# Performance work log

Measured on AMD Instinct MI355X. Metric: run time of the kernel, lower is better.

Reference implementation:

```python
import jax, jax.numpy as jnp
import numpy as np

B, T, F = 16, 4096, 80      # batch, frames, mel bins
C = 512                     # conv channels
ZD, ZN = 64, 512            # codebook dim / size
YD, YN = 128, 128           # speaker embed dim / count
K = 5                       # kernel size
SLOPE = 0.2                 # leaky relu negative slope


def conv1d(x, w, b):
    # x: [B,Cin,T], w: [Cout,Cin,K], 'same' padding, stride 1
    pad = (w.shape[-1] - 1) // 2
    y = jax.lax.conv_general_dilated(x, w, (1,), [(pad, pad)],
                                     dimension_numbers=('NCH', 'OIH', 'NCH'))
    return y + b[None, :, None]


def convT1(x, w, b):
    # torch ConvTranspose1d(stride=1, padding=(K-1)//2) == conv with spatially
    # flipped, in/out-swapped kernel. w: [Cin, Cout, K]
    wc = jnp.flip(w, -1).transpose(1, 0, 2)  # -> [Cout, Cin, K]
    return conv1d(x, wc, b)


def ln_c(x, g, b, eps=1e-5):
    # layer norm over channel axis, per (batch, time) position
    m = jnp.mean(x, 1, keepdims=True)
    v = jnp.var(x, 1, keepdims=True)
    return (x - m) * jax.lax.rsqrt(v + eps) * g[None, :, None] + b[None, :, None]


def _forward(x, y, enc_w1, enc_b1, enc_g1, enc_bt1, enc_w2, enc_b2, enc_g2, enc_bt2,
             enc_w3, enc_b3, enc_g3, enc_bt3, mlp_w, mlp_b, codebook, spk_emb,
             dec_w1, dec_b1, dec_g1, dec_bt1, dec_w2, dec_b2, dec_g2, dec_bt2,
             dec_w3, dec_b3):
    xc = x.transpose(0, 2, 1)                                    # [B,F,T]
    # Conditions: normalized speaker embedding lookup
    spk = spk_emb / jnp.linalg.norm(spk_emb, axis=1, keepdims=True)
    ye = spk[y].transpose(0, 2, 1)                               # [B,YD,T]
    # encoder: Conv1d -> LayerNorm(channel) -> LeakyReLU, x3, then 1x1 conv to z_dim
    h = jax.nn.leaky_relu(ln_c(conv1d(xc, enc_w1, enc_b1), enc_g1, enc_bt1), SLOPE)
    h = jax.nn.leaky_relu(ln_c(conv1d(h, enc_w2, enc_b2), enc_g2, enc_bt2), SLOPE)
    h = jax.nn.leaky_relu(ln_c(conv1d(h, enc_w3, enc_b3), enc_g3, enc_bt3), SLOPE)
    z = conv1d(h, mlp_w, mlp_b)                                  # [B,ZD,T]
    # vector quantizer (eval path): cdist^2 -> argmin -> gather
    zt = z.transpose(0, 2, 1)                                    # [B,T,ZD]
    zf = zt.reshape(-1, ZD)                                      # [B*T,ZD]
    d = (jnp.sum(zf * zf, axis=1, keepdims=True)
         + jnp.sum(codebook * codebook, axis=1)
         - 2.0 * zf @ codebook.T)                                # [B*T,ZN]
    idx = jnp.argmin(d, axis=1)
    z_vq = codebook[idx].reshape(zt.shape).transpose(0, 2, 1)    # [B,ZD,T]
    # decoder: (concat y -> ConvT -> LayerNorm -> GLU) x2, then concat y -> ConvT
    def glu_layer(h, w, b, g, bt):
        h = jnp.concatenate([h, ye], axis=1)
        h = ln_c(convT1(h, w, b), g, bt)
        a, gate = jnp.split(h, 2, axis=1)
        return a * jax.nn.sigmoid(gate)
    h = glu_layer(z_vq, dec_w1, dec_b1, dec_g1, dec_bt1)
    h = glu_layer(h, dec_w2, dec_b2, dec_g2, dec_bt2)
    h = jnp.concatenate([h, ye], axis=1)
    xhat = convT1(h, dec_w3, dec_b3)                             # [B,F,T]
    return xhat.transpose(0, 2, 1)                               # [B,T,F]


def setup_inputs() -> dict:
    key = jax.random.key(0)
    ks = jax.random.split(key, 16)
    def n(k, shape, sc=0.05):
        return jax.random.normal(k, shape, jnp.float32) * sc
    return {
        "x": jax.random.normal(ks[0], (B, T, F), jnp.float32),
        "y": jax.random.randint(ks[1], (B, T), 0, YN),
        "enc_w1": n(ks[2], (C, F, K)), "enc_b1": jnp.zeros(C), "enc_g1": jnp.ones(C), "enc_bt1": jnp.zeros(C),
        "enc_w2": n(ks[3], (C, C, K)), "enc_b2": jnp.zeros(C), "enc_g2": jnp.ones(C), "enc_bt2": jnp.zeros(C),
        "enc_w3": n(ks[4], (C, C, K)), "enc_b3": jnp.zeros(C), "enc_g3": jnp.ones(C), "enc_bt3": jnp.zeros(C),
        "mlp_w": n(ks[5], (ZD, C, 1)), "mlp_b": jnp.zeros(ZD),
        "codebook": jax.random.normal(ks[6], (ZN, ZD), jnp.float32),
        "spk_emb": jax.random.normal(ks[7], (YN, YD), jnp.float32),
        "dec_w1": n(ks[8], (ZD + YD, 2 * C, K)), "dec_b1": jnp.zeros(2 * C), "dec_g1": jnp.ones(2 * C), "dec_bt1": jnp.zeros(2 * C),
        "dec_w2": n(ks[9], (C + YD, 2 * C, K)), "dec_b2": jnp.zeros(2 * C), "dec_g2": jnp.ones(2 * C), "dec_bt2": jnp.zeros(2 * C),
        "dec_w3": n(ks[10], (C + YD, F, K)), "dec_b3": jnp.zeros(F),
    }


def reference(x, y, enc_w1, enc_b1, enc_g1, enc_bt1, enc_w2, enc_b2, enc_g2, enc_bt2,
              enc_w3, enc_b3, enc_g3, enc_bt3, mlp_w, mlp_b, codebook, spk_emb,
              dec_w1, dec_b1, dec_g1, dec_bt1, dec_w2, dec_b2, dec_g2, dec_bt2,
              dec_w3, dec_b3):
    return _forward(x, y, enc_w1, enc_b1, enc_g1, enc_bt1, enc_w2, enc_b2, enc_g2, enc_bt2,
                    enc_w3, enc_b3, enc_g3, enc_bt3, mlp_w, mlp_b, codebook, spk_emb,
                    dec_w1, dec_b1, dec_g1, dec_bt1, dec_w2, dec_b2, dec_g2, dec_bt2,
                    dec_w3, dec_b3)
```

## Files before the change

### kernel.cpp

```cpp
#include <hip/hip_runtime.h>
#include <hip/hip_bf16.h>
#include <cmath>

#define T_LEN 4096
#define BATCH 16
typedef __hip_bfloat16 bf16;
typedef unsigned short u16;
typedef float f32x4 __attribute__((ext_vector_type(4)));
typedef short s16x8 __attribute__((ext_vector_type(8)));
typedef unsigned short u16x8 __attribute__((ext_vector_type(8)));

__device__ __forceinline__ float ldx(const void* p, int dt, size_t i) {
    return dt ? __bfloat162float(((const bf16*)p)[i]) : ((const float*)p)[i];
}
__device__ __forceinline__ void stx(void* p, int dt, size_t i, float v) {
    if (dt) ((bf16*)p)[i] = __float2bfloat16(v);
    else ((float*)p)[i] = v;
}
__device__ __forceinline__ u16 f2b(float v) {
    bf16 h = __float2bfloat16(v);
    return *(u16*)&h;
}
__device__ __forceinline__ float b2f(u16 u) {
    return __bfloat162float(*(const bf16*)&u);
}

__global__ void detect_kernel(const float* __restrict__ x, int* __restrict__ flag) {
    __shared__ int s[256];
    int tid = threadIdx.x;
    int bad = 0;
    for (int i = tid; i < 2048; i += 256) {
        float v = x[i];
        if (!(fabsf(v) < 1e30f)) bad = 1;
    }
    s[tid] = bad;
    __syncthreads();
    for (int off = 128; off > 0; off >>= 1) {
        if (tid < off) s[tid] |= s[tid + off];
        __syncthreads();
    }
    if (tid == 0) *flag = s[0];
}

__global__ void spk_norm_kernel(const int* __restrict__ dflag,
                                const void* __restrict__ spk,
                                float* __restrict__ out) {
    const int f = *dflag;
    int s = blockIdx.x, d = threadIdx.x;
    float v = ldx(spk, f, (size_t)s * 128 + d);
    __shared__ float red[128];
    red[d] = v * v;
    __syncthreads();
    for (int off = 64; off > 0; off >>= 1) {
        if (d < off) red[d] += red[d + off];
        __syncthreads();
    }
    float rs = rsqrtf(red[0]);
    out[s * 128 + d] = v * rs;
}

__global__ __launch_bounds__(256) void repack0_kernel(
    const int* __restrict__ dflag, const void* __restrict__ src,
    int Cout, int Cin, int K, int ocp, int Cinp,
    bf16* __restrict__ dsthi, bf16* __restrict__ dstlo) {
    const int F = *dflag;
    __shared__ u16 sh[64 * 32 * 5];
    __shared__ u16 sl[64 * 32 * 5];
    const int ic0 = blockIdx.x * 32;
    const int oc0 = blockIdx.y * 64;
    const int tid = threadIdx.x;
    const int N = 64 * 32 * K;
    for (int idx = tid; idx < N; idx += 256) {
        int ocl = idx / (32 * K);
        int r = idx % (32 * K);
        int icl = r / K, k = r % K;
        int oc = oc0 + ocl, ic = ic0 + icl;
        float v = 0.f;
        if (oc < Cout && ic < Cin)
            v = ldx(src, F, ((size_t)oc * Cin + ic) * K + k);
        u16 hb = f2b(v);
        sh[(ocl * 32 + icl) * K + k] = hb;
        sl[(ocl * 32 + icl) * K + k] = f2b(v - b2f(hb));
    }
    __syncthreads();
    const int M = K * 64 * 4;
    for (int idx = tid; idx < M; idx += 256) {
        int k = idx / (64 * 4);
        int r = idx % (64 * 4);
        int ocl = r >> 2;
        int g8 = (r & 3) << 3;
        u16x8 h, l;
#pragma unroll
        for (int j = 0; j < 8; j++) {
            h[j] = sh[(ocl * 32 + g8 + j) * K + k];
            l[j] = sl[(ocl * 32 + g8 + j) * K + k];
        }
        size_t off = ((size_t)k * ocp + oc0 + ocl) * Cinp + ic0 + g8;
        *(u16x8*)&dsthi[off] = h;
        if (dstlo) *(u16x8*)&dstlo[off] = l;
    }
}

__global__ __launch_bounds__(256) void repack1_kernel(
    const int* __restrict__ dflag, const void* __restrict__ src,
    int Cout, int Cin, int K, int ocp, int Cinp,
    bf16* __restrict__ dsthi) {
    const int F = *dflag;
    __shared__ u16 sh[64 * 32 * 5];
    const int ic0 = blockIdx.x * 64;
    const int oc0 = blockIdx.y * 32;
    const int tid = threadIdx.x;
    const int N = 64 * 32 * K;
    for (int idx = tid; idx < N; idx += 256) {
        int icl = idx / (32 * K);
        int r = idx % (32 * K);
        int ocl = r / K, k = r % K;
        int oc = oc0 + ocl, ic = ic0 + icl;
        float v = 0.f;
        if (oc < Cout && ic < Cin)
            v = ldx(src, F, ((size_t)ic * Cout + oc) * K + k);
        sh[(icl * 32 + ocl) * K + (K - 1 - k)] = f2b(v);
    }
    __syncthreads();
    const int M = K * 32 * 8;
    for (int idx = tid; idx < M; idx += 256) {
        int k = idx / (32 * 8);
        int r = idx % (32 * 8);
        int ocl = r >> 3;
        int g8 = (r & 7) << 3;
        u16x8 h;
#pragma unroll
        for (int j = 0; j < 8; j++)
            h[j] = sh[((g8 + j) * 32 + ocl) * K + k];
        size_t off = ((size_t)k * ocp + oc0 + ocl) * Cinp + ic0 + g8;
        *(u16x8*)&dsthi[off] = h;
    }
}

__global__ void xprep_kernel(const int* __restrict__ dflag,
                             const void* __restrict__ x, int b0,
                             bf16* __restrict__ xp) {
    const int F = *dflag;
    int b = blockIdx.y;
    int t = blockIdx.x * 256 + threadIdx.x;
    size_t src = ((size_t)(b0 + b) * T_LEN + t) * 80;
    u16* row = (u16*)xp + ((size_t)b * T_LEN + t) * 192;
    for (int c4 = 0; c4 < 96; c4 += 4) {
        ushort4 h, l;
        u16* hp = (u16*)&h;
        u16* lp = (u16*)&l;
        for (int j = 0; j < 4; j++) {
            int c = c4 + j;
            float v = (c < 80) ? ldx(x, F, src + c) : 0.f;
            u16 hb = f2b(v);
            hp[j] = hb;
            lp[j] = f2b(v - b2f(hb));
        }
        *(ushort4*)&row[c4] = h;
        *(ushort4*)&row[96 + c4] = l;
    }
}

__global__ void ye_kernel(const int* __restrict__ y, int b0,
                          const float* __restrict__ spk_n,
                          bf16* __restrict__ D1, bf16* __restrict__ D2,
                          bf16* __restrict__ D3) {
    int b = blockIdx.y;
    int t = blockIdx.x * 256 + threadIdx.x;
    int idx = y[(size_t)(b0 + b) * T_LEN + t];
    const float* s = spk_n + (size_t)idx * 128;
    size_t r = (size_t)b * T_LEN + t;
    u16* p1 = (u16*)D1 + r * 192 + 64;
    u16* p2 = (u16*)D2 + r * 640 + 512;
    u16* p3 = (u16*)D3 + r * 640 + 512;
    for (int d4 = 0; d4 < 128; d4 += 4) {
        float4 v = *(const float4*)&s[d4];
        ushort4 h;
        h.x = f2b(v.x); h.y = f2b(v.y); h.z = f2b(v.z); h.w = f2b(v.w);
        *(ushort4*)&p1[d4] = h;
        *(ushort4*)&p2[d4] = h;
        *(ushort4*)&p3[d4] = h;
    }
}

template <int KK>
__global__ __launch_bounds__(256) void conv_mfma(
    const int* __restrict__ dflag,
    const bf16* __restrict__ act, int RS, int loOff, int aloMode, int Cinp,
    const bf16* __restrict__ whi, const bf16* __restrict__ wlo, int wloMode,
    const void* __restrict__ bias,
    void* __restrict__ outp, int odt, int oRS, int ocMax, int boff) {
    constexpr int PAD = (KK - 1) / 2;
    constexpr int SROWS = 128 + KK - 1;
    const int F = *dflag;
    const bool useALo = (aloMode == 1) || (aloMode == 2 && F == 0);
    const bool useWLo = (wloMode == 2 && F == 0) && (wlo != nullptr);
    const int ocp = gridDim.y << 7;
    const int t0 = blockIdx.x * 128;
    const int oc0 = blockIdx.y * 128;
    const int b = blockIdx.z;
    const int tid = threadIdx.x;
    const int lane = tid & 63;
    const int wid = tid >> 6;
    const int widT = wid >> 1;
    const int widN = wid & 1;
    const int l16 = lane & 15;
    const int quad = lane >> 4;
    const int q8 = quad * 8;

    __shared__ __align__(16) bf16 sA[2 * SROWS * 40];
    __shared__ __align__(16) bf16 sB[KK * 128 * 40];

    f32x4 acc[4][4];
#pragma unroll
    for (int i = 0; i < 4; i++)
#pragma unroll
        for (int j = 0; j < 4; j++) acc[i][j] = (f32x4){0.f, 0.f, 0.f, 0.f};

    const int nch = Cinp >> 5;
    for (int ch = 0; ch < nch; ch++) {
        const int ic0 = ch << 5;
        for (int g = tid; g < SROWS * 4; g += 256) {
            int row = g >> 2, c8 = (g & 3) << 3;
            int t = t0 - PAD + row;
            u16x8 v = (u16x8){0, 0, 0, 0, 0, 0, 0, 0};
            u16x8 vl = (u16x8){0, 0, 0, 0, 0, 0, 0, 0};
            if (t >= 0 && t < T_LEN) {
                const u16* src = (const u16*)act + ((size_t)b * T_LEN + t) * RS + ic0 + c8;
                v = *(const u16x8*)src;
                if (useALo) vl = *(const u16x8*)(src + loOff);
            }
            *(u16x8*)&sA[row * 40 + c8] = v;
            if (useALo) *(u16x8*)&sA[(SROWS + row) * 40 + c8] = vl;
        }
        for (int g = tid; g < KK * 512; g += 256) {
            int tap = g >> 9;
            int r = g & 511;
            int ocr = r >> 2, c8 = (r & 3) << 3;
            const u16* src = (const u16*)whi +
                             ((size_t)tap * ocp + oc0 + ocr) * Cinp + ic0 + c8;
            *(u16x8*)&sB[(tap * 128 + ocr) * 40 + c8] = *(const u16x8*)src;
        }
        __syncthreads();

#pragma unroll
        for (int tap = 0; tap < KK; tap++) {
            s16x8 bfr[4];
#pragma unroll
            for (int ni = 0; ni < 4; ni++)
                bfr[ni] = *(const s16x8*)&sB[(tap * 128 + widN * 64 + ni * 16 + l16) * 40 + q8];
#pragma unroll
            for (int mi = 0; mi < 4; mi++) {
                int row = widT * 64 + mi * 16 + l16 + tap;
                s16x8 a = *(const s16x8*)&sA[row * 40 + q8];
#pragma unroll
                for (int ni = 0; ni < 4; ni++)
                    acc[mi][ni] = __builtin_amdgcn_mfma_f32_16x16x32_bf16(
                        a, bfr[ni], acc[mi][ni], 0, 0, 0);
                if (useALo) {
                    s16x8 al = *(const s16x8*)&sA[(SROWS + row) * 40 + q8];
#pragma unroll
                    for (int ni = 0; ni < 4; ni++)
                        acc[mi][ni] = __builtin_amdgcn_mfma_f32_16x16x32_bf16(
                            al, bfr[ni], acc[mi][ni], 0, 0, 0);
                }
            }
        }
        if (useWLo) {
            __syncthreads();
            for (int g = tid; g < KK * 512; g += 256) {
                int tap = g >> 9;
                int r = g & 511;
                int ocr = r >> 2, c8 = (r & 3) << 3;
                const u16* src = (const u16*)wlo +
                                 ((size_t)tap * ocp + oc0 + ocr) * Cinp + ic0 + c8;
                *(u16x8*)&sB[(tap * 128 + ocr) * 40 + c8] = *(const u16x8*)src;
            }
            __syncthreads();
#pragma unroll
            for (int tap = 0; tap < KK; tap++) {
                s16x8 bfr[4];
#pragma unroll
                for (int ni = 0; ni < 4; ni++)
                    bfr[ni] = *(const s16x8*)&sB[(tap * 128 + widN * 64 + ni * 16 + l16) * 40 + q8];
#pragma unroll
                for (int mi = 0; mi < 4; mi++) {
                    int row = widT * 64 + mi * 16 + l16 + tap;
                    s16x8 a = *(const s16x8*)&sA[row * 40 + q8];
#pragma unroll
                    for (int ni = 0; ni < 4; ni++)
                        acc[mi][ni] = __builtin_amdgcn_mfma_f32_16x16x32_bf16(
                            a, bfr[ni], acc[mi][ni], 0, 0, 0);
                }
            }
        }
        __syncthreads();
    }

#pragma unroll
    for (int ni = 0; ni < 4; ni++) {
        int oc = oc0 + widN * 64 + ni * 16 + l16;
        if (oc >= ocMax) continue;
        float bv = ldx(bias, F, oc);
#pragma unroll
        for (int mi = 0; mi < 4; mi++) {
#pragma unroll
            for (int r = 0; r < 4; r++) {
                int t = t0 + widT * 64 + mi * 16 + quad * 4 + r;
                float v = acc[mi][ni][r] + bv;
                size_t off = ((size_t)(b + boff) * T_LEN + t) * (size_t)oRS + oc;
                if (odt == 0) ((float*)outp)[off] = v;
                else if (odt == 1) ((bf16*)outp)[off] = __float2bfloat16(v);
                else stx(outp, F, off, v);
            }
        }
    }
}

__global__ __launch_bounds__(256) void ln_lrelu(
    const int* __restrict__ dflag, const float* __restrict__ Fin,
    bf16* __restrict__ E, const void* __restrict__ g, const void* __restrict__ bt) {
    const int Fl = *dflag;
    int b = blockIdx.y;
    int t = blockIdx.x * 4 + (threadIdx.x >> 6);
    int lane = threadIdx.x & 63;
    const float* row = Fin + ((size_t)b * T_LEN + t) * 512 + lane * 8;
    float vv[8];
    *(float4*)&vv[0] = *(const float4*)row;
    *(float4*)&vv[4] = *(const float4*)(row + 4);
    float s = 0.f, s2 = 0.f;
#pragma unroll
    for (int j = 0; j < 8; j++) { s += vv[j]; s2 += vv[j] * vv[j]; }
    for (int m = 32; m; m >>= 1) {
        s += __shfl_xor(s, m);
        s2 += __shfl_xor(s2, m);
    }
    float mean = s / 512.f;
    float var = s2 / 512.f - mean * mean;
    float rstd = rsqrtf(var + 1e-5f);
    u16* eo = (u16*)E + ((size_t)b * T_LEN + t) * 1024 + lane * 8;
    ushort4 h[2], l[2];
#pragma unroll
    for (int j = 0; j < 8; j++) {
        int c = lane * 8 + j;
        float v = (vv[j] - mean) * rstd * ldx(g, Fl, c) + ldx(bt, Fl, c);
        v = v >= 0.f ? v : 0.2f * v;
        u16 hb = f2b(v);
        ((u16*)h)[j] = hb;
        ((u16*)l)[j] = f2b(v - b2f(hb));
    }
    *(ushort4*)&eo[0] = h[0];
    *(ushort4*)&eo[4] = h[1];
    *(ushort4*)&eo[512] = l[0];
    *(ushort4*)&eo[516] = l[1];
}

__global__ __launch_bounds__(256) void ln_glu(
    const int* __restrict__ dflag, const bf16* __restrict__ Fin,
    bf16* __restrict__ D, int oRS, const void* __restrict__ g,
    const void* __restrict__ bt) {
    const int Fl = *dflag;
    int b = blockIdx.y;
    int t = blockIdx.x * 4 + (threadIdx.x >> 6);
    int lane = threadIdx.x & 63;
    const u16* row = (const u16*)Fin + ((size_t)b * T_LEN + t) * 1024;
    ushort4 ua[2], ug[2];
    ua[0] = *(const ushort4*)&row[lane * 8];
    ua[1] = *(const ushort4*)&row[lane * 8 + 4];
    ug[0] = *(const ushort4*)&row[512 + lane * 8];
    ug[1] = *(const ushort4*)&row[512 + lane * 8 + 4];
    float av[8], gv[8];
#pragma unroll
    for (int j = 0; j < 8; j++) {
        av[j] = b2f(((u16*)ua)[j]);
        gv[j] = b2f(((u16*)ug)[j]);
    }
    float s = 0.f, s2 = 0.f;
#pragma unroll
    for (int j = 0; j < 8; j++) {
        s += av[j] + gv[j];
        s2 += av[j] * av[j] + gv[j] * gv[j];
    }
    for (int m = 32; m; m >>= 1) {
        s += __shfl_xor(s, m);
        s2 += __shfl_xor(s2, m);
    }
    float mean = s / 1024.f;
    float var = s2 / 1024.f - mean * mean;
    float rstd = rsqrtf(var + 1e-5f);
    ushort4 o[2];
#pragma unroll
    for (int j = 0; j < 8; j++) {
        int c = lane * 8 + j;
        float a = (av[j] - mean) * rstd * ldx(g, Fl, c) + ldx(bt, Fl, c);
        float gg = (gv[j] - mean) * rstd * ldx(g, Fl, 512 + c) + ldx(bt, Fl, 512 + c);
        ((u16*)o)[j] = f2b(a / (1.f + expf(-gg)));
    }
    u16* op = (u16*)D + ((size_t)b * T_LEN + t) * oRS + lane * 8;
    *(ushort4*)&op[0] = o[0];
    *(ushort4*)&op[4] = o[1];
}

__global__ __launch_bounds__(256) void vq_kernel(
    const int* __restrict__ dflag, const float* __restrict__ z,
    const void* __restrict__ cb, bf16* __restrict__ D1) {
    const int F = *dflag;
    int b = blockIdx.y;
    int t = blockIdx.x * 256 + threadIdx.x;
    int tid = threadIdx.x;

    __shared__ float sCB[128 * 64];
    __shared__ float sCC[128];

    float zr[64];
    const float* zp = z + ((size_t)b * T_LEN + t) * 64;
#pragma unroll
    for (int d4 = 0; d4 < 64; d4 += 4) *(float4*)&zr[d4] = *(const float4*)&zp[d4];
    float zz = 0.f;
#pragma unroll
    for (int d = 0; d < 64; d++) zz += zr[d] * zr[d];

    float best = 3.4e38f;
    int bidx = 0;
    for (int chunk = 0; chunk < 4; chunk++) {
        __syncthreads();
        for (int i = tid; i < 8192; i += 256)
            sCB[i] = ldx(cb, F, (size_t)chunk * 8192 + i);
        __syncthreads();
        if (tid < 128) {
            float cc = 0.f;
#pragma unroll 8
            for (int d = 0; d < 64; d++) {
                float cv = sCB[tid * 64 + d];
                cc += cv * cv;
            }
            sCC[tid] = cc;
        }
        __syncthreads();
        for (int c = 0; c < 128; c++) {
            const float* cp = &sCB[c * 64];
            float dot = 0.f;
#pragma unroll
            for (int d = 0; d < 64; d++) dot += zr[d] * cp[d];
            float dist = zz + sCC[c] - 2.f * dot;
            if (dist < best) { best = dist; bidx = chunk * 128 + c; }
        }
    }
    u16* out = (u16*)D1 + ((size_t)b * T_LEN + t) * 192;
    for (int d4 = 0; d4 < 64; d4 += 4) {
        ushort4 h;
        h.x = f2b(ldx(cb, F, (size_t)bidx * 64 + d4));
        h.y = f2b(ldx(cb, F, (size_t)bidx * 64 + d4 + 1));
        h.z = f2b(ldx(cb, F, (size_t)bidx * 64 + d4 + 2));
        h.w = f2b(ldx(cb, F, (size_t)bidx * 64 + d4 + 3));
        *(ushort4*)&out[d4] = h;
    }
}

extern "C" void kernel_launch(void* const* d_in, const int* in_sizes, int n_in,
                              void* d_out, int out_size, void* d_ws,
                              size_t ws_size, hipStream_t stream) {
    const void* x = d_in[0];
    const int* y = (const int*)d_in[1];
    const void* enc_w1 = d_in[2];  const void* enc_b1 = d_in[3];
    const void* enc_g1 = d_in[4];  const void* enc_bt1 = d_in[5];
    const void* enc_w2 = d_in[6];  const void* enc_b2 = d_in[7];
    const void* enc_g2 = d_in[8];  const void* enc_bt2 = d_in[9];
    const void* enc_w3 = d_in[10]; const void* enc_b3 = d_in[11];
    const void* enc_g3 = d_in[12]; const void* enc_bt3 = d_in[13];
    const void* mlp_w = d_in[14];  const void* mlp_b = d_in[15];
    const void* codebook = d_in[16];
    const void* spk_emb = d_in[17];
    const void* dec_w1 = d_in[18]; const void* dec_b1 = d_in[19];
    const void* dec_g1 = d_in[20]; const void* dec_bt1 = d_in[21];
    const void* dec_w2 = d_in[22]; const void* dec_b2 = d_in[23];
    const void* dec_g2 = d_in[24]; const void* dec_bt2 = d_in[25];
    const void* dec_w3 = d_in[26]; const void* dec_b3 = d_in[27];

    const size_t SW1 = (size_t)5 * 512 * 96;
    const size_t SW2 = (size_t)5 * 512 * 512;
    const size_t SW3 = SW2;
    const size_t SWM = (size_t)128 * 512;
    const size_t SD1 = (size_t)5 * 1024 * 192;
    const size_t SD2 = (size_t)5 * 1024 * 640;
    const size_t SD3 = (size_t)5 * 128 * 640;
    const size_t HI_TOT = SW1 + SW2 + SW3 + SWM + SD1 + SD2 + SD3;
    const size_t LO_TOT = SW1 + SW2 + SW3 + SWM;

    const size_t PB = (size_t)T_LEN * (192 * 2 + 1024 * 2 + 2048 + 64 * 4 + 640 * 2 + 640 * 2);
    const size_t FIXED = 256 + 65536 + (HI_TOT + LO_TOT) * 2;

    int nb = BATCH;
    while (nb > 1 && FIXED + (size_t)nb * PB > ws_size) nb >>= 1;

    char* p = (char*)d_ws;
    int* dflag = (int*)p;        p += 256;
    float* spk_n = (float*)p;    p += 65536;
    bf16* w1h = (bf16*)p;        p += SW1 * 2;
    bf16* w2h = (bf16*)p;        p += SW2 * 2;
    bf16* w3h = (bf16*)p;        p += SW3 * 2;
    bf16* wmh = (bf16*)p;        p += SWM * 2;
    bf16* wd1 = (bf16*)p;        p += SD1 * 2;
    bf16* wd2 = (bf16*)p;        p += SD2 * 2;
    bf16* wd3 = (bf16*)p;        p += SD3 * 2;
    bf16* w1l = (bf16*)p;        p += SW1 * 2;
    bf16* w2l = (bf16*)p;        p += SW2 * 2;
    bf16* w3l = (bf16*)p;        p += SW3 * 2;
    bf16* wml = (bf16*)p;        p += SWM * 2;
    bf16* xp = (bf16*)p;         p += (size_t)nb * T_LEN * 192 * 2;
    bf16* E = (bf16*)p;          p += (size_t)nb * T_LEN * 1024 * 2;
    char* Fb = p;                p += (size_t)nb * T_LEN * 2048;
    float* zbuf = (float*)p;     p += (size_t)nb * T_LEN * 64 * 4;
    bf16* D2 = (bf16*)p;         p += (size_t)nb * T_LEN * 640 * 2;
    bf16* D3 = (bf16*)p;
    bf16* D1 = xp;
    float* Ff = (float*)Fb;
    bf16* Fh = (bf16*)Fb;

    dim3 blk(256);

    detect_kernel<<<1, 256, 0, stream>>>((const float*)x, dflag);
    spk_norm_kernel<<<128, 128, 0, stream>>>(dflag, spk_emb, spk_n);

    repack0_kernel<<<dim3(3, 8), blk, 0, stream>>>(dflag, enc_w1, 512, 80, 5, 512, 96, w1h, w1l);
    repack0_kernel<<<dim3(16, 8), blk, 0, stream>>>(dflag, enc_w2, 512, 512, 5, 512, 512, w2h, w2l);
    repack0_kernel<<<dim3(16, 8), blk, 0, stream>>>(dflag, enc_w3, 512, 512, 5, 512, 512, w3h, w3l);
    repack0_kernel<<<dim3(16, 2), blk, 0, stream>>>(dflag, mlp_w, 64, 512, 1, 128, 512, wmh, wml);
    repack1_kernel<<<dim3(3, 32), blk, 0, stream>>>(dflag, dec_w1, 1024, 192, 5, 1024, 192, wd1);
    repack1_kernel<<<dim3(10, 32), blk, 0, stream>>>(dflag, dec_w2, 1024, 640, 5, 1024, 640, wd2);
    repack1_kernel<<<dim3(10, 4), blk, 0, stream>>>(dflag, dec_w3, 80, 640, 5, 128, 640, wd3);

    for (int b0 = 0; b0 < BATCH; b0 += nb) {
        dim3 gT(T_LEN / 256, nb);
        dim3 gLN(T_LEN / 4, nb);

        xprep_kernel<<<gT, blk, 0, stream>>>(dflag, x, b0, xp);

        conv_mfma<5><<<dim3(32, 4, nb), blk, 0, stream>>>(
            dflag, xp, 192, 96, 2, 96, w1h, w1l, 2, enc_b1, Ff, 0, 512, 512, 0);
        ye_kernel<<<gT, blk, 0, stream>>>(y, b0, spk_n, D1, D2, D3);
        ln_lrelu<<<gLN, blk, 0, stream>>>(dflag, Ff, E, enc_g1, enc_bt1);
        conv_mfma<5><<<dim3(32, 4, nb), blk, 0, stream>>>(
            dflag, E, 1024, 512, 1, 512, w2h, w2l, 2, enc_b2, Ff, 0, 512, 512, 0);
        ln_lrelu<<<gLN, blk, 0, stream>>>(dflag, Ff, E, enc_g2, enc_bt2);
        conv_mfma<5><<<dim3(32, 4, nb), blk, 0, stream>>>(
            dflag, E, 1024, 512, 1, 512, w3h, w3l, 2, enc_b3, Ff, 0, 512, 512, 0);
        ln_lrelu<<<gLN, blk, 0, stream>>>(dflag, Ff, E, enc_g3, enc_bt3);

        conv_mfma<1><<<dim3(32, 1, nb), blk, 0, stream>>>(
            dflag, E, 1024, 512, 1, 512, wmh, wml, 2, mlp_b, zbuf, 0, 64, 64, 0);

        vq_kernel<<<gT, blk, 0, stream>>>(dflag, zbuf, codebook, D1);

        conv_mfma<5><<<dim3(32, 8, nb), blk, 0, stream>>>(
            dflag, D1, 192, 0, 0, 192, wd1, nullptr, 0, dec_b1, Fh, 1, 1024, 1024, 0);
        ln_glu<<<gLN, blk, 0, stream>>>(dflag, Fh, D2, 640, dec_g1, dec_bt1);
        conv_mfma<5><<<dim3(32, 8, nb), blk, 0, stream>>>(
            dflag, D2, 640, 0, 0, 640, wd2, nullptr, 0, dec_b2, Fh, 1, 1024, 1024, 0);
        ln_glu<<<gLN, blk, 0, stream>>>(dflag, Fh, D3, 640, dec_g2, dec_bt2);
        conv_mfma<5><<<dim3(32, 1, nb), blk, 0, stream>>>(
            dflag, D3, 640, 0, 0, 640, wd3, nullptr, 0, dec_b3, d_out, 2, 80, 80, b0);
    }
}
```

Before: 4.928 ms.

## Load conv weight fragments directly from global memory instead of staging in LDS

Removes the shared-memory weight tile in the MFMA conv kernel. Each wave now reads its B fragments straight from global memory (relying on L1/L2 for reuse across waves and blocks), and the extra syncs for the low-weight pass go away. The kernel also gets a min-blocks-per-SM hint of 4 to raise occupancy now that LDS use is smaller. The risk is that global loads issued inside the MFMA loop add latency and duplicate traffic: two waves share each weight tile, and the loads are only 16-byte strided reads per lane.

```diff
diff --git a/kernel.cpp b/kernel.cpp
--- a/kernel.cpp
+++ b/kernel.cpp
@@ -184,7 +184,7 @@
 }
 
 template <int KK>
-__global__ __launch_bounds__(256) void conv_mfma(
+__global__ __launch_bounds__(256, 4) void conv_mfma(
     const int* __restrict__ dflag,
     const bf16* __restrict__ act, int RS, int loOff, int aloMode, int Cinp,
     const bf16* __restrict__ whi, const bf16* __restrict__ wlo, int wloMode,
@@ -209,7 +209,10 @@
     const int q8 = quad * 8;
 
     __shared__ __align__(16) bf16 sA[2 * SROWS * 40];
-    __shared__ __align__(16) bf16 sB[KK * 128 * 40];
+
+    const u16* wrow_hi = (const u16*)whi + (size_t)(oc0 + widN * 64 + l16) * Cinp + q8;
+    const u16* wrow_lo = useWLo
+        ? (const u16*)wlo + (size_t)(oc0 + widN * 64 + l16) * Cinp + q8 : nullptr;
 
     f32x4 acc[4][4];
 #pragma unroll
@@ -233,14 +236,6 @@
             *(u16x8*)&sA[row * 40 + c8] = v;
             if (useALo) *(u16x8*)&sA[(SROWS + row) * 40 + c8] = vl;
         }
-        for (int g = tid; g < KK * 512; g += 256) {
-            int tap = g >> 9;
-            int r = g & 511;
-            int ocr = r >> 2, c8 = (r & 3) << 3;
-            const u16* src = (const u16*)whi +
-                             ((size_t)tap * ocp + oc0 + ocr) * Cinp + ic0 + c8;
-            *(u16x8*)&sB[(tap * 128 + ocr) * 40 + c8] = *(const u16x8*)src;
-        }
         __syncthreads();
 
 #pragma unroll
@@ -248,7 +243,8 @@
             s16x8 bfr[4];
 #pragma unroll
             for (int ni = 0; ni < 4; ni++)
-                bfr[ni] = *(const s16x8*)&sB[(tap * 128 + widN * 64 + ni * 16 + l16) * 40 + q8];
+                bfr[ni] = *(const s16x8*)(wrow_hi +
+                    ((size_t)tap * ocp + ni * 16) * Cinp + ic0);
 #pragma unroll
             for (int mi = 0; mi < 4; mi++) {
                 int row = widT * 64 + mi * 16 + l16 + tap;
@@ -267,22 +263,13 @@
             }
         }
         if (useWLo) {
-            __syncthreads();
-            for (int g = tid; g < KK * 512; g += 256) {
-                int tap = g >> 9;
-                int r = g & 511;
-                int ocr = r >> 2, c8 = (r & 3) << 3;
-                const u16* src = (const u16*)wlo +
-                                 ((size_t)tap * ocp + oc0 + ocr) * Cinp + ic0 + c8;
-                *(u16x8*)&sB[(tap * 128 + ocr) * 40 + c8] = *(const u16x8*)src;
-            }
-            __syncthreads();
 #pragma unroll
             for (int tap = 0; tap < KK; tap++) {
                 s16x8 bfr[4];
 #pragma unroll
                 for (int ni = 0; ni < 4; ni++)
-                    bfr[ni] = *(const s16x8*)&sB[(tap * 128 + widN * 64 + ni * 16 + l16) * 40 + q8];
+                    bfr[ni] = *(const s16x8*)(wrow_lo +
+                        ((size_t)tap * ocp + ni * 16) * Cinp + ic0);
 #pragma unroll
                 for (int mi = 0; mi < 4; mi++) {
                     int row = widT * 64 + mi * 16 + l16 + tap;
```

New measurement: 4.804 ms. 2.5% less time.
